# Kernel optimization log

Hardware: AMD Instinct MI355X
Metric: run time of the kernel (lower is better)

Reference implementation:

```python
import jax, jax.numpy as jnp
import numpy as np

H = W = 64            # grid resolution (input image HxW)
N = H * W
T = 25                # landscape sample points
K_MAX = 2             # landscape levels
M0 = 0.05             # DTM mass parameter
LIMS = [[224.0, 0.0], [0.0, 224.0]]
T_MIN, T_MAX = 0.0, 45.0   # fixed tseq covering the DTM value range for this grid scale


def _grid_coords():
    gx = np.linspace(LIMS[0][0], LIMS[0][1], H)
    gy = np.linspace(LIMS[1][0], LIMS[1][1], W)
    X, Y = np.meshgrid(gx, gy, indexing='ij')
    return np.stack([X.ravel(), Y.ravel()], 1).astype(np.float32)  # [N,2]


def _grid_edges():
    idx = np.arange(N).reshape(H, W)
    e_h = np.stack([idx[:, :-1].ravel(), idx[:, 1:].ravel()], 1)
    e_v = np.stack([idx[:-1, :].ravel(), idx[1:, :].ravel()], 1)
    return np.concatenate([e_h, e_v], 0).astype(np.int32)  # [E,2] 4-connectivity


def dtm(w):
    """Weighted (robust) distance-to-measure on the fixed grid, r=2. w: [B,N] >=0."""
    coords = jnp.asarray(_grid_coords())
    diff = coords[:, None, :] - coords[None, :, :]
    d2 = jnp.sum(diff * diff, -1)                      # [N,N] squared distances
    idx = jnp.argsort(d2, axis=1)                      # fixed nearest-neighbor order
    d2s = jnp.take_along_axis(d2, idx, axis=1)         # [N,N]
    wsort = w[:, idx]                                  # [B,N,N] weights in distance order
    cumw = jnp.cumsum(wsort, -1)
    thr = M0 * jnp.sum(w, -1)[:, None, None]           # [B,1,1] target mass
    # fractional mass contribution of each neighbor until cumulative mass hits thr
    eff = jnp.clip(thr - (cumw - wsort), 0.0, wsort)
    return jnp.sqrt(jnp.sum(eff * d2s, -1) / thr[..., 0])  # [B,N]


def ph0(f, edges):
    """0-dim sublevel persistence of vertex function f on the grid graph (elder rule)."""
    u, v = edges[:, 0], edges[:, 1]
    wgt = jnp.maximum(f[u], f[v])          # edge filtration values
    es = edges[jnp.argsort(wgt)]

    def step(label, e):
        eu, ev = e[0], e[1]
        ru, rv = label[eu], label[ev]
        bu, bv = f[ru], f[rv]
        u_elder = (bu < bv) | ((bu == bv) & (ru <= rv))
        elder = jnp.where(u_elder, ru, rv)
        younger = jnp.where(u_elder, rv, ru)
        merge = ru != rv
        birth = f[younger]
        death = jnp.maximum(f[eu], f[ev])
        label = jnp.where(merge & (label == younger), elder, label)
        return label, (birth, death, merge)

    label0 = jnp.arange(N, dtype=jnp.int32)
    _, (b, d, valid) = jax.lax.scan(step, label0, es)
    # essential class: global min, killed at max filtration value
    b = jnp.concatenate([b, f.min()[None]])
    d = jnp.concatenate([d, f.max()[None]])
    valid = jnp.concatenate([valid, jnp.array([True])])
    return b, d, valid


def landscape(b, d, valid, tseq):
    # tent functions: [P,T]
    tri = jnp.minimum(tseq[None, :] - b[:, None], d[:, None] - tseq[None, :])
    tri = jnp.where(valid[:, None], jnp.maximum(tri, 0.0), 0.0)
    top = jax.lax.top_k(tri.T, K_MAX)[0]   # [T, K_MAX]
    return top.T.reshape(-1)               # [K_MAX*T]


def reference(input, Wg, bg, Wfc, bfc):
    B = input.shape[0]
    w = input.reshape(B, -1)               # Flatten: pixel weights on the grid
    f = dtm(w)                             # [B,N] DTM filtration
    edges = jnp.asarray(_grid_edges())
    b, d, valid = jax.vmap(lambda fi: ph0(fi, edges))(f)
    tseq = jnp.linspace(T_MIN, T_MAX, T, dtype=jnp.float32)
    land = jax.vmap(lambda bi, di, vi: landscape(bi, di, vi, tseq))(b, d, valid)  # [B,50]
    x = land @ Wg.T + bg                   # learned g_theta -> out_features
    signal = jnp.abs(jax.lax.stop_gradient(x)).sum(0)
    output = jnp.maximum(x, 0.0) @ Wfc.T + bfc
    return output, signal


def setup_inputs() -> dict:
    key = jax.random.key(0)
    k1, k2, k3 = jax.random.split(key, 3)
    B = 2
    return {
        'input': jax.random.uniform(k1, (B, 1, H, W), dtype=jnp.float32),
        'Wg': 0.1 * jax.random.normal(k2, (50, K_MAX * T), dtype=jnp.float32),
        'bg': jnp.zeros((50,), jnp.float32),
        'Wfc': 0.1 * jax.random.normal(k3, (10, 50), dtype=jnp.float32),
        'bfc': jnp.zeros((10,), jnp.float32),
    }
```

## Files before the change

kernel.cpp:

```cpp
#include <hip/hip_runtime.h>

#define NPTS 4096
#define NEDGE 8064
#define M0f 0.05f
#define KMAXD2 7938
#define IDCAP 90
#define SORTCAP 512
#define PAIRCAP 160

typedef unsigned long long u64;

__device__ inline float waveSum(float x) {
  for (int m = 32; m >= 1; m >>= 1) x += __shfl_xor(x, m);
  return x;
}

__device__ inline int isqrt_i(int x) {
  int r = (int)sqrtf((float)x);
  if ((r + 1) * (r + 1) <= x) r++;
  else if (r * r > x) r--;
  return r;
}

__device__ inline int rdl(int v, int l) { return __builtin_amdgcn_readlane(v, l); }
__device__ inline float rdlf(float v, int l) {
  return __uint_as_float((unsigned)__builtin_amdgcn_readlane((int)__float_as_uint(v), l));
}
__device__ inline u64 rdl64(u64 x, int l) {
  unsigned lo = (unsigned)__builtin_amdgcn_readlane((int)(unsigned)(x & 0xffffffffull), l);
  unsigned hi = (unsigned)__builtin_amdgcn_readlane((int)(unsigned)(x >> 32), l);
  return ((u64)hi << 32) | (u64)lo;
}
__device__ inline int sel2(int v0, int v1, int idx) {
  int x0 = __shfl(v0, idx & 63);
  int x1 = __shfl(v1, idx & 63);
  return (idx < 64) ? x0 : x1;
}
__device__ inline u64 shfl_xor64(u64 x, int m) {
  int lo = __shfl_xor((int)(unsigned)(x & 0xffffffffull), m);
  int hi = __shfl_xor((int)(unsigned)(x >> 32), m);
  return ((u64)(unsigned)hi << 32) | (u64)(unsigned)lo;
}

#define CXL(R, J, K) { \
  u64 vo = shfl_xor64(e##R, J); \
  bool up = (((((R) * 64) & (K)) | (lane & (K))) == 0); \
  bool lower = ((lane & (J)) == 0); \
  bool kmin = (lower == up); \
  u64 mn = (e##R < vo) ? e##R : vo; \
  u64 mx = (e##R < vo) ? vo : e##R; \
  e##R = kmin ? mn : mx; }
#define ALL2(J, K) CXL(0,J,K) CXL(1,J,K)
#define CXR(RA, RB, K) { \
  const bool up = ((((RA) * 64) & (K)) == 0); \
  u64 va = e##RA, vb = e##RB; \
  u64 mn = (va < vb) ? va : vb; \
  u64 mx = (va < vb) ? vb : va; \
  e##RA = up ? mn : mx; e##RB = up ? mx : mn; }

__global__ __launch_bounds__(1024) void dtm_kernel(const float* __restrict__ win,
                                                   float* __restrict__ fout,
                                                   float* __restrict__ out) {
  __shared__ float P0[64][65];
  __shared__ float P1[64][65];
  __shared__ float P2[64][65];
  int b = blockIdx.y;
  const float* w = win + b * NPTS;
  int tid = threadIdx.x, lane = tid & 63, wv = tid >> 6;

  if (blockIdx.x == 0 && blockIdx.y == 0 && tid < 50) out[20 + tid] = 0.f;

  for (int rr = 0; rr < 4; ++rr) {
    int r = (wv << 2) | rr;
    float x0 = w[(r << 6) | lane];
    float fl = (float)lane;
    float x1 = x0 * fl, x2 = x1 * fl;
    for (int d = 1; d < 64; d <<= 1) {
      float t0 = __shfl_up(x0, d);
      float t1 = __shfl_up(x1, d);
      float t2 = __shfl_up(x2, d);
      if (lane >= d) { x0 += t0; x1 += t1; x2 += t2; }
    }
    P0[r][lane] = x0; P1[r][lane] = x1; P2[r][lane] = x2;
  }
  __syncthreads();

  float sumw = waveSum(P0[lane][63]);
  float thr = M0f * sumw;

  int q = blockIdx.x * 16 + wv;
  int qi = q >> 6, qj = q & 63;
  int di = qi - lane;
  int disq = di * di;

  auto evalF = [&](int K) -> float {
    float s0 = 0.f;
    int rem = K - disq;
    if (rem >= 0) {
      int r = isqrt_i(rem);
      int l0 = qj - r; l0 = l0 < 0 ? 0 : l0;
      int h0 = qj + r; h0 = h0 > 63 ? 63 : h0;
      s0 = P0[lane][h0] - (l0 > 0 ? P0[lane][l0 - 1] : 0.f);
    }
    return waveSum(s0);
  };

  int lo = -1, hi = 256;
  float Flo = 0.f;
  for (;;) {
    float F = evalF(hi);
    if (F >= thr || hi == KMAXD2) break;
    lo = hi; Flo = F;
    hi = (hi == 256) ? 1024 : KMAXD2;
  }
  while (hi - lo > 1) {
    int mid = (lo + hi) >> 1;
    float F = evalF(mid);
    if (F >= thr) hi = mid; else { lo = mid; Flo = F; }
  }
  int kstar = hi;
  float Fm = Flo;

  float g = 0.f;
  {
    int rem = (kstar - 1) - disq;
    if (rem >= 0) {
      int r = isqrt_i(rem);
      int l0 = qj - r; l0 = l0 < 0 ? 0 : l0;
      int h0 = qj + r; h0 = h0 > 63 ? 63 : h0;
      float S0 = P0[lane][h0] - (l0 > 0 ? P0[lane][l0 - 1] : 0.f);
      float S1 = P1[lane][h0] - (l0 > 0 ? P1[lane][l0 - 1] : 0.f);
      float S2 = P2[lane][h0] - (l0 > 0 ? P2[lane][l0 - 1] : 0.f);
      float fq = (float)qj;
      g = (float)disq * S0 + fq * fq * S0 - 2.f * fq * S1 + S2;
    }
  }
  float G = waveSum(g);
  float val = (G + (thr - Fm) * (float)kstar) / thr;
  val = val < 0.f ? 0.f : val;
  float res = (224.f / 63.f) * sqrtf(val);
  if (lane == 0) fout[b * NPTS + q] = res;
}

__global__ __launch_bounds__(1024) void ph_fused(const float* __restrict__ fin,
                                                 const float* __restrict__ Wg,
                                                 const float* __restrict__ bg,
                                                 const float* __restrict__ Wfc,
                                                 const float* __restrict__ bfc,
                                                 float* __restrict__ out) {
  __shared__ float sf[NPTS];
  __shared__ __align__(16) int srep[NPTS];
  __shared__ __align__(16) int sbasin[NPTS];
  __shared__ float smu[128];
  __shared__ int sminv[128];
  __shared__ float2 spairs[PAIRCAP];
  __shared__ float sland[50];
  __shared__ float sx[50];
  __shared__ float sWg[2500];
  __shared__ float sbg[50];
  __shared__ float sWfc[500];
  __shared__ float sbfc[10];
  __shared__ int comparr[128];
  __shared__ unsigned minW[128], minI[128];
  __shared__ u64 mstlist[128];
  __shared__ int c_m, c_l2, c_np, c_hook;
  __shared__ unsigned fminb, fmaxb;

  int b = blockIdx.x;
  int tid = threadIdx.x;
  int lane = tid & 63;
  if (tid == 0) { c_m = 0; c_l2 = 0; c_np = 0; fminb = 0x7f800000u; fmaxb = 0u; }
  if (tid < 128) { smu[tid] = 3.0e38f; sminv[tid] = tid; mstlist[tid] = ~0ull; }

  for (int i = tid; i < 2500; i += 1024) sWg[i] = Wg[i];
  for (int i = tid; i < 500; i += 1024) sWfc[i] = Wfc[i];
  if (tid < 50) sbg[tid] = bg[tid];
  if (tid >= 64 && tid < 74) sbfc[tid - 64] = bfc[tid - 64];

  {
    float lmin = 3.0e38f, lmax = 0.f;
    for (int v = tid; v < NPTS; v += 1024) {
      float x = fin[b * NPTS + v];
      sf[v] = x;
      lmin = fminf(lmin, x);
      lmax = fmaxf(lmax, x);
    }
    for (int m = 32; m >= 1; m >>= 1) {
      lmin = fminf(lmin, __shfl_xor(lmin, m));
      lmax = fmaxf(lmax, __shfl_xor(lmax, m));
    }
    if (lane == 0) {
      atomicMin(&fminb, __float_as_uint(lmin));
      atomicMax(&fmaxb, __float_as_uint(lmax));
    }
  }
  __syncthreads();

  int preg[4];
#pragma unroll 4
  for (int s = 0; s < 4; ++s) {
    int v = tid + s * 1024;
    int vi = v >> 6, vj = v & 63;
    float bf = sf[v]; int bi = v;
    if (vj > 0)  { float fn = sf[v - 1];  int n = v - 1;  if (fn < bf || (fn == bf && n < bi)) { bf = fn; bi = n; } }
    if (vj < 63) { float fn = sf[v + 1];  int n = v + 1;  if (fn < bf || (fn == bf && n < bi)) { bf = fn; bi = n; } }
    if (vi > 0)  { float fn = sf[v - 64]; int n = v - 64; if (fn < bf || (fn == bf && n < bi)) { bf = fn; bi = n; } }
    if (vi < 63) { float fn = sf[v + 64]; int n = v + 64; if (fn < bf || (fn == bf && n < bi)) { bf = fn; bi = n; } }
    srep[v] = bi;
    preg[s] = bi;
  }
  __syncthreads();

  for (int it = 0; it < 8; ++it) {
#pragma unroll 4
    for (int s = 0; s < 4; ++s) {
      int x = srep[preg[s]];
      x = srep[x];
      srep[tid + s * 1024] = x;
      preg[s] = x;
    }
    __syncthreads();
  }

  for (int v = tid; v < NPTS; v += 1024) {
    if (srep[v] == v) {
      int id = atomicAdd(&c_m, 1);
      if (id < IDCAP) { sbasin[v] = id; smu[id] = sf[v]; sminv[id] = v; }
      else sbasin[v] = IDCAP - 1;
    }
  }
  __syncthreads();
  for (int v = tid; v < NPTS; v += 1024) {
    if (srep[v] != v) sbasin[v] = sbasin[srep[v]];
  }
  __syncthreads();

  unsigned* ptable = (unsigned*)srep;
  for (int i = tid; i < 4096; i += 1024) ptable[i] = 0xFFFFFFFFu;
  __syncthreads();
  for (int e = tid; e < NEDGE; e += 1024) {
    int u, v2;
    if (e < 4032) { int i = e / 63; int j = e - i * 63; u = (i << 6) | j; v2 = u + 1; }
    else          { int e2 = e - 4032; u = e2; v2 = u + 64; }
    int bu = sbasin[u], bv = sbasin[v2];
    if (bu != bv) {
      float wgt = fmaxf(sf[u], sf[v2]);
      int a = bu < bv ? bu : bv, bb2 = bu < bv ? bv : bu;
      int t = (bb2 * (bb2 - 1)) / 2 + a;
      atomicMin(&ptable[t], __float_as_uint(wgt));
    }
  }
  __syncthreads();

  u64* slist2 = (u64*)sbasin;
  for (int t = tid; t < 4096; t += 1024) {
    unsigned wv2 = ptable[t];
    if (wv2 != 0xFFFFFFFFu) {
      int bb2 = (int)((1.0f + sqrtf(1.0f + 8.0f * (float)t)) * 0.5f);
      while (bb2 > 1 && (bb2 * (bb2 - 1)) / 2 > t) bb2--;
      while (((bb2 + 1) * bb2) / 2 <= t) bb2++;
      int aa = t - (bb2 * (bb2 - 1)) / 2;
      int slot = atomicAdd(&c_l2, 1);
      if (slot < SORTCAP) slist2[slot] = ((u64)wv2 << 32) | (unsigned)((bb2 << 8) | aa);
    }
  }
  __syncthreads();
  int n2 = c_l2; if (n2 > SORTCAP) n2 = SORTCAP;

  int comp0 = lane, comp1 = 64 + lane;
  int nmst = 0;
  for (int round = 0; round < 8; ++round) {
    if (tid < 64) {
      comparr[lane] = comp0; comparr[64 + lane] = comp1;
      minW[lane] = 0xFFFFFFFFu; minW[64 + lane] = 0xFFFFFFFFu;
      minI[lane] = 0xFFFFFFFFu; minI[64 + lane] = 0xFFFFFFFFu;
      if (lane == 0) c_hook = 0;
    }
    __syncthreads();
    for (int e = tid; e < n2; e += 1024) {
      u64 ev = slist2[e];
      int a = (int)(ev & 0xffull), bb2 = (int)((ev >> 8) & 0xffull);
      int ra = comparr[a], rb = comparr[bb2];
      if (ra != rb) {
        unsigned w = (unsigned)(ev >> 32);
        atomicMin(&minW[ra], w);
        atomicMin(&minW[rb], w);
      }
    }
    __syncthreads();
    for (int e = tid; e < n2; e += 1024) {
      u64 ev = slist2[e];
      int a = (int)(ev & 0xffull), bb2 = (int)((ev >> 8) & 0xffull);
      int ra = comparr[a], rb = comparr[bb2];
      if (ra != rb) {
        unsigned w = (unsigned)(ev >> 32);
        if (w == minW[ra]) atomicMin(&minI[ra], (unsigned)e);
        if (w == minW[rb]) atomicMin(&minI[rb], (unsigned)e);
      }
    }
    __syncthreads();
    if (tid < 64) {
      unsigned mi0 = minI[lane], mi1 = minI[64 + lane];
      u64 ev0 = (mi0 != 0xFFFFFFFFu) ? slist2[mi0] : 0ull;
      u64 ev1 = (mi1 != 0xFFFFFFFFu) ? slist2[mi1] : 0ull;
      int a0 = (int)(ev0 & 0xffull), b0 = (int)((ev0 >> 8) & 0xffull);
      int a1 = (int)(ev1 & 0xffull), b1 = (int)((ev1 >> 8) & 0xffull);
      int raA = sel2(comp0, comp1, a0), rbA = sel2(comp0, comp1, b0);
      int raB = sel2(comp0, comp1, a1), rbB = sel2(comp0, comp1, b1);
      int parA0 = (mi0 != 0xFFFFFFFFu) ? ((raA == lane) ? rbA : raA) : lane;
      int parA1 = (mi1 != 0xFFFFFFFFu) ? ((raB == 64 + lane) ? rbB : raB) : (64 + lane);
      int pp0 = sel2(parA0, parA1, parA0);
      int pp1 = sel2(parA0, parA1, parA1);
      int par0 = (pp0 == lane && lane < parA0) ? lane : parA0;
      int par1 = (pp1 == (64 + lane) && (64 + lane) < parA1) ? (64 + lane) : parA1;
      bool h0 = (par0 != lane);
      bool h1 = (par1 != (64 + lane));
      u64 mlo = __ballot(h0);
      int cnt0 = __popcll(mlo);
      int pos0 = nmst + __popcll(mlo & ((1ull << lane) - 1ull));
      if (h0 && pos0 < 128) mstlist[pos0] = ev0;
      u64 mhi = __ballot(h1);
      int pos1 = nmst + cnt0 + __popcll(mhi & ((1ull << lane) - 1ull));
      if (h1 && pos1 < 128) mstlist[pos1] = ev1;
      int tot = cnt0 + __popcll(mhi);
      nmst += tot;
      if (lane == 0 && tot > 0) c_hook = 1;
      for (int j = 0; j < 8; ++j) {
        int n0 = sel2(par0, par1, par0);
        int n1 = sel2(par0, par1, par1);
        bool ch = (n0 != par0) || (n1 != par1);
        par0 = n0; par1 = n1;
        if (__ballot(ch) == 0ull) break;
      }
      comp0 = sel2(par0, par1, comp0);
      comp1 = sel2(par0, par1, comp1);
    }
    __syncthreads();
    if (c_hook == 0) break;
  }

  if (tid < 64) {
    u64 e0 = mstlist[lane], e1 = mstlist[64 + lane];
    ALL2(1,2)
    ALL2(2,4) ALL2(1,4)
    ALL2(4,8) ALL2(2,8) ALL2(1,8)
    ALL2(8,16) ALL2(4,16) ALL2(2,16) ALL2(1,16)
    ALL2(16,32) ALL2(8,32) ALL2(4,32) ALL2(2,32) ALL2(1,32)
    ALL2(32,64) ALL2(16,64) ALL2(8,64) ALL2(4,64) ALL2(2,64) ALL2(1,64)
    CXR(0,1,128)
    ALL2(32,128) ALL2(16,128) ALL2(8,128) ALL2(4,128) ALL2(2,128) ALL2(1,128)

    int p0 = lane, p1 = 64 + lane;
    float m0 = smu[lane], m1 = smu[64 + lane];
    int r0 = sminv[lane], r1 = sminv[64 + lane];
    int np = 0;
    for (int s = 0; s < nmst; ++s) {
      u64 ev = (s < 64) ? rdl64(e0, s) : rdl64(e1, s - 64);
      int a = (int)(ev & 0xffull), bb2 = (int)((ev >> 8) & 0xffull);
      unsigned wb = (unsigned)(ev >> 32);
      int ia = a & 63, ib = bb2 & 63;
      int pa = (a < 64) ? rdl(p0, ia) : rdl(p1, ia);
      int pb = (bb2 < 64) ? rdl(p0, ib) : rdl(p1, ib);
      if (pa == pb) continue;
      float ma = (a < 64) ? rdlf(m0, ia) : rdlf(m1, ia);
      float mb = (bb2 < 64) ? rdlf(m0, ib) : rdlf(m1, ib);
      int ra = (a < 64) ? rdl(r0, ia) : rdl(r1, ia);
      int rb = (bb2 < 64) ? rdl(r0, ib) : rdl(r1, ib);
      bool aeld = (ma < mb) || (ma == mb && ra <= rb);
      int eld = aeld ? pa : pb, yng = aeld ? pb : pa;
      float m_e = aeld ? ma : mb; int r_e = aeld ? ra : rb;
      float byoung = aeld ? mb : ma;
      bool g0 = (p0 == yng), g1 = (p1 == yng);
      p0 = g0 ? eld : p0; m0 = g0 ? m_e : m0; r0 = g0 ? r_e : r0;
      p1 = g1 ? eld : p1; m1 = g1 ? m_e : m1; r1 = g1 ? r_e : r1;
      if (lane == 0 && np < PAIRCAP - 1) spairs[np] = make_float2(byoung, __uint_as_float(wb));
      np++;
    }
    if (np > PAIRCAP - 1) np = PAIRCAP - 1;
    if (lane == 0) {
      spairs[np] = make_float2(__uint_as_float(fminb), __uint_as_float(fmaxb));
      c_np = np + 1;
    }
  }
  __syncthreads();

  int totp = c_np;
  if (tid < 25) {
    float tv = 1.875f * (float)tid;
    float top1 = 0.f, top2 = 0.f;
    for (int i = 0; i < totp; ++i) {
      float2 p = spairs[i];
      float tri = fminf(tv - p.x, p.y - tv);
      tri = fmaxf(tri, 0.f);
      if (tri > top1) { top2 = top1; top1 = tri; }
      else if (tri > top2) top2 = tri;
    }
    sland[tid] = top1;
    sland[25 + tid] = top2;
  }
  __syncthreads();

  if (tid < 50) {
    float acc = sbg[tid];
    for (int k = 0; k < 50; ++k) acc += sland[k] * sWg[tid * 50 + k];
    sx[tid] = acc;
  }
  __syncthreads();

  if (tid < 50) atomicAdd(&out[20 + tid], fabsf(sx[tid]));
  if (tid >= 64 && tid < 74) {
    int c = tid - 64;
    float acc = sbfc[c];
    for (int o = 0; o < 50; ++o) acc += fmaxf(sx[o], 0.f) * sWfc[c * 50 + o];
    out[b * 10 + c] = acc;
  }
}

extern "C" void kernel_launch(void* const* d_in, const int* in_sizes, int n_in,
                              void* d_out, int out_size, void* d_ws, size_t ws_size,
                              hipStream_t stream) {
  (void)in_sizes; (void)n_in; (void)out_size; (void)ws_size;
  const float* input = (const float*)d_in[0];
  const float* Wg  = (const float*)d_in[1];
  const float* bg  = (const float*)d_in[2];
  const float* Wfc = (const float*)d_in[3];
  const float* bfc = (const float*)d_in[4];
  float* out = (float*)d_out;

  float* f_ws = (float*)d_ws;

  dtm_kernel<<<dim3(256, 2), 1024, 0, stream>>>(input, f_ws, out);
  ph_fused<<<dim3(2), 1024, 0, stream>>>(f_ws, Wg, bg, Wfc, bfc, out);
}
```

Before: 65.77 us.

## Pack Boruvka min-edge into 64-bit atomic, early-exit pointer jumping, vectorize loads

Merges the two-pass weight-then-index atomicMin in the Boruvka MST rounds into a single 64-bit packed key atomicMin, removing one pass over the edges and one barrier per round. It adds a ballot-based convergence check so the pointer-jumping loop for basin labels exits early. Global loads of the filtration, Wg and Wfc now use float4. Round caps drop from 8 to 7, which could leave components unmerged on unusual inputs.

```diff
diff --git a/kernel.cpp b/kernel.cpp
--- a/kernel.cpp
+++ b/kernel.cpp
@@ -148,7 +148,7 @@
                                                  const float* __restrict__ Wfc,
                                                  const float* __restrict__ bfc,
                                                  float* __restrict__ out) {
-  __shared__ float sf[NPTS];
+  __shared__ __align__(16) float sf[NPTS];
   __shared__ __align__(16) int srep[NPTS];
   __shared__ __align__(16) int sbasin[NPTS];
   __shared__ float smu[128];
@@ -156,35 +156,33 @@
   __shared__ float2 spairs[PAIRCAP];
   __shared__ float sland[50];
   __shared__ float sx[50];
-  __shared__ float sWg[2500];
+  __shared__ __align__(16) float sWg[2500];
   __shared__ float sbg[50];
-  __shared__ float sWfc[500];
+  __shared__ __align__(16) float sWfc[500];
   __shared__ float sbfc[10];
   __shared__ int comparr[128];
-  __shared__ unsigned minW[128], minI[128];
+  __shared__ u64 minKey[128];
   __shared__ u64 mstlist[128];
-  __shared__ int c_m, c_l2, c_np, c_hook;
+  __shared__ int c_m, c_np, c_hook, c_chg;
   __shared__ unsigned fminb, fmaxb;
+  __shared__ int c_l2;
 
   int b = blockIdx.x;
   int tid = threadIdx.x;
   int lane = tid & 63;
-  if (tid == 0) { c_m = 0; c_l2 = 0; c_np = 0; fminb = 0x7f800000u; fmaxb = 0u; }
+  if (tid == 0) { c_m = 0; c_l2 = 0; c_np = 0; c_chg = 0; fminb = 0x7f800000u; fmaxb = 0u; }
   if (tid < 128) { smu[tid] = 3.0e38f; sminv[tid] = tid; mstlist[tid] = ~0ull; }
 
-  for (int i = tid; i < 2500; i += 1024) sWg[i] = Wg[i];
-  for (int i = tid; i < 500; i += 1024) sWfc[i] = Wfc[i];
+  if (tid < 625) ((float4*)sWg)[tid] = ((const float4*)Wg)[tid];
+  if (tid < 125) ((float4*)sWfc)[tid] = ((const float4*)Wfc)[tid];
   if (tid < 50) sbg[tid] = bg[tid];
   if (tid >= 64 && tid < 74) sbfc[tid - 64] = bfc[tid - 64];
 
   {
-    float lmin = 3.0e38f, lmax = 0.f;
-    for (int v = tid; v < NPTS; v += 1024) {
-      float x = fin[b * NPTS + v];
-      sf[v] = x;
-      lmin = fminf(lmin, x);
-      lmax = fmaxf(lmax, x);
-    }
+    float4 v4 = ((const float4*)(fin + b * NPTS))[tid];
+    ((float4*)sf)[tid] = v4;
+    float lmin = fminf(fminf(v4.x, v4.y), fminf(v4.z, v4.w));
+    float lmax = fmaxf(fmaxf(v4.x, v4.y), fmaxf(v4.z, v4.w));
     for (int m = 32; m >= 1; m >>= 1) {
       lmin = fminf(lmin, __shfl_xor(lmin, m));
       lmax = fmaxf(lmax, __shfl_xor(lmax, m));
@@ -212,14 +210,19 @@
   __syncthreads();
 
   for (int it = 0; it < 8; ++it) {
+    bool ch = false;
 #pragma unroll 4
     for (int s = 0; s < 4; ++s) {
       int x = srep[preg[s]];
       x = srep[x];
+      ch |= (x != preg[s]);
       srep[tid + s * 1024] = x;
       preg[s] = x;
     }
+    u64 bl = __ballot(ch);
+    if (lane == 0 && bl != 0ull) c_chg = it + 1;
     __syncthreads();
+    if (c_chg != it + 1) break;
   }
 
   for (int v = tid; v < NPTS; v += 1024) {
@@ -269,38 +272,28 @@
 
   int comp0 = lane, comp1 = 64 + lane;
   int nmst = 0;
-  for (int round = 0; round < 8; ++round) {
+  for (int round = 0; round < 7; ++round) {
     if (tid < 64) {
       comparr[lane] = comp0; comparr[64 + lane] = comp1;
-      minW[lane] = 0xFFFFFFFFu; minW[64 + lane] = 0xFFFFFFFFu;
-      minI[lane] = 0xFFFFFFFFu; minI[64 + lane] = 0xFFFFFFFFu;
       if (lane == 0) c_hook = 0;
     }
+    if (tid < 128) minKey[tid] = ~0ull;
     __syncthreads();
     for (int e = tid; e < n2; e += 1024) {
       u64 ev = slist2[e];
       int a = (int)(ev & 0xffull), bb2 = (int)((ev >> 8) & 0xffull);
       int ra = comparr[a], rb = comparr[bb2];
       if (ra != rb) {
-        unsigned w = (unsigned)(ev >> 32);
-        atomicMin(&minW[ra], w);
-        atomicMin(&minW[rb], w);
-      }
-    }
-    __syncthreads();
-    for (int e = tid; e < n2; e += 1024) {
-      u64 ev = slist2[e];
-      int a = (int)(ev & 0xffull), bb2 = (int)((ev >> 8) & 0xffull);
-      int ra = comparr[a], rb = comparr[bb2];
-      if (ra != rb) {
-        unsigned w = (unsigned)(ev >> 32);
-        if (w == minW[ra]) atomicMin(&minI[ra], (unsigned)e);
-        if (w == minW[rb]) atomicMin(&minI[rb], (unsigned)e);
+        u64 key = (ev & 0xFFFFFFFF00000000ull) | (u64)(unsigned)e;
+        atomicMin(&minKey[ra], key);
+        atomicMin(&minKey[rb], key);
       }
     }
     __syncthreads();
     if (tid < 64) {
-      unsigned mi0 = minI[lane], mi1 = minI[64 + lane];
+      u64 k0 = minKey[lane], k1 = minKey[64 + lane];
+      unsigned mi0 = (k0 != ~0ull) ? (unsigned)(k0 & 0xffffffffull) : 0xFFFFFFFFu;
+      unsigned mi1 = (k1 != ~0ull) ? (unsigned)(k1 & 0xffffffffull) : 0xFFFFFFFFu;
       u64 ev0 = (mi0 != 0xFFFFFFFFu) ? slist2[mi0] : 0ull;
       u64 ev1 = (mi1 != 0xFFFFFFFFu) ? slist2[mi1] : 0ull;
       int a0 = (int)(ev0 & 0xffull), b0 = (int)((ev0 >> 8) & 0xffull);
@@ -325,12 +318,12 @@
       int tot = cnt0 + __popcll(mhi);
       nmst += tot;
       if (lane == 0 && tot > 0) c_hook = 1;
-      for (int j = 0; j < 8; ++j) {
+      for (int j = 0; j < 7; ++j) {
         int n0 = sel2(par0, par1, par0);
         int n1 = sel2(par0, par1, par1);
-        bool ch = (n0 != par0) || (n1 != par1);
+        bool chp = (n0 != par0) || (n1 != par1);
         par0 = n0; par1 = n1;
-        if (__ballot(ch) == 0ull) break;
+        if (__ballot(chp) == 0ull) break;
       }
       comp0 = sel2(par0, par1, comp0);
       comp1 = sel2(par0, par1, comp1);
```

Result: faster. 62.85 us (-4.4%).
